# Kernel optimization log

Measured on AMD Instinct MI355X. Metric: run time of the kernel, lower is better.

The kernel has to match this reference:

```python
import jax, jax.numpy as jnp
import numpy as np

LAMDA = 1.0  # init arg: weight on uniformity term
ALIGN_ALPHA = 2.0
UNIF_T = 2.0
EPS = 1e-12


def _l2_normalize(x):
    # F.normalize(x, dim=1): x / max(||x||, eps)
    n = jnp.sqrt(jnp.sum(x * x, axis=1, keepdims=True))
    return x / jnp.maximum(n, EPS)


def _lalign(q, k):
    # mean over batch of ||q_i - k_i||_2 ^ alpha (alpha=2 -> squared distance)
    d2 = jnp.sum((q - k) ** 2, axis=1)
    return jnp.mean(d2)


def _lunif(x):
    # log( mean_{i<j} exp(-t * ||x_i - x_j||^2) )
    # x is unit-norm, so ||x_i - x_j||^2 = 2 - 2 <x_i, x_j>
    n = x.shape[0]
    sq = jnp.maximum(2.0 - 2.0 * (x @ x.T), 0.0)            # [N, N] squared dists
    iu = jnp.triu(jnp.ones((n, n), dtype=bool), k=1)        # strict upper: i < j pairs
    vals = jnp.where(iu, jnp.exp(-UNIF_T * sq), 0.0)
    npairs = jnp.asarray(n * (n - 1) // 2, dtype=x.dtype)
    return jnp.log(vals.sum() / npairs)


def setup_inputs() -> dict:
    key = jax.random.key(0)
    kq, kk = jax.random.split(key)
    q = jax.random.normal(kq, (8192, 128), dtype=jnp.float32)
    k = jax.random.normal(kk, (8192, 128), dtype=jnp.float32)
    return {"q": q, "k": k}


def reference(q, k):
    qn = _l2_normalize(q)
    kn = _l2_normalize(k)
    align = _lalign(qn, kn)
    uniform = (_lunif(qn) + _lunif(kn)) / 2.0
    return align + LAMDA * uniform
```

## Files before the change

### kernel.cpp

```cpp
#include <hip/hip_runtime.h>
#include <math.h>

#define NROWS 8192
#define DIM   128
#define NT    64
#define TRI   2080

typedef __attribute__((ext_vector_type(8))) __bf16 bf16x8;
typedef __attribute__((ext_vector_type(4))) float  f32x4;
typedef __attribute__((ext_vector_type(2))) float  f32x2;

__device__ __forceinline__ unsigned short f2bf(float f) {
    unsigned int u = __float_as_uint(f);
    u += 0x7fffu + ((u >> 16) & 1u);
    return (unsigned short)(u >> 16);
}

__device__ __forceinline__ void gload_lds16(const uint4* g, uint4* l) {
    __builtin_amdgcn_global_load_lds(
        (const __attribute__((address_space(1))) uint32_t*)
            (const __attribute__((address_space(1))) void*)g,
        (__attribute__((address_space(3))) uint32_t*)
            (__attribute__((address_space(3))) void*)l,
        16, 0, 0);
}

__global__ __launch_bounds__(256) void norm_kernel(
        const float* __restrict__ q, const float* __restrict__ k,
        unsigned int* __restrict__ qn, unsigned int* __restrict__ kn,
        float* __restrict__ align_part) {
    int wave = threadIdx.x >> 6;
    int lane = threadIdx.x & 63;
    int row  = blockIdx.x * 4 + wave;

    const float2 qv = reinterpret_cast<const float2*>(q)[row * 64 + lane];
    const float2 kv = reinterpret_cast<const float2*>(k)[row * 64 + lane];

    float sq = qv.x * qv.x + qv.y * qv.y;
    float sk = kv.x * kv.x + kv.y * kv.y;
    #pragma unroll
    for (int off = 32; off; off >>= 1) {
        sq += __shfl_xor(sq, off);
        sk += __shfl_xor(sk, off);
    }
    float qi = 1.0f / fmaxf(sqrtf(sq), 1e-12f);
    float ki = 1.0f / fmaxf(sqrtf(sk), 1e-12f);
    float qx = qv.x * qi, qy = qv.y * qi;
    float kx = kv.x * ki, ky = kv.y * ki;

    qn[row * 64 + lane] = (unsigned int)f2bf(qx) | ((unsigned int)f2bf(qy) << 16);
    kn[row * 64 + lane] = (unsigned int)f2bf(kx) | ((unsigned int)f2bf(ky) << 16);

    float dx = qx - kx, dy = qy - ky;
    float d2 = dx * dx + dy * dy;
    #pragma unroll
    for (int off = 32; off; off >>= 1) d2 += __shfl_xor(d2, off);

    __shared__ float red[4];
    if (lane == 0) red[wave] = d2;
    __syncthreads();
    if (threadIdx.x == 0)
        align_part[blockIdx.x] = red[0] + red[1] + red[2] + red[3];
}

__global__ __launch_bounds__(512) void gram_kernel(
        const uint4* __restrict__ qn, const uint4* __restrict__ kn,
        float* __restrict__ unif_part) {
    __shared__ uint4 lds[4096];
    __shared__ float red[8];

    int bid = blockIdx.x;
    int mat = 0, t = bid;
    if (t >= TRI) { mat = 1; t -= TRI; }
    int ti = 0, rem = t;
    while (rem >= NT - ti) { rem -= NT - ti; ++ti; }
    int tj = ti + rem;
    const uint4* __restrict__ x = mat ? kn : qn;

    int tid = threadIdx.x;
    int wid = tid >> 6, lane = tid & 63;

    {
        int lrow4 = lane >> 4;
        int sw    = lane & 15;
        #pragma unroll
        for (int it = 0; it < 8; ++it) {
            int inst = wid * 8 + it;
            int r    = inst * 4 + lrow4;
            int rr   = r & 127;
            int tile = (r < 128) ? ti : tj;
            int s    = sw ^ (rr & 15);
            gload_lds16(&x[((size_t)tile * 128 + rr) * 16 + s], &lds[inst * 64]);
        }
    }
    __syncthreads();

    int wr = wid >> 2, wc = wid & 3;
    int lr = lane & 15, lg = lane >> 4;

    f32x4 c[4][2];
    #pragma unroll
    for (int m = 0; m < 4; ++m)
        #pragma unroll
        for (int n = 0; n < 2; ++n)
            c[m][n] = (f32x4){0.f, 0.f, 0.f, 0.f};

    #pragma unroll
    for (int ks = 0; ks < 4; ++ks) {
        int slot = ks * 4 + lg;
        bf16x8 a[4], b[2];
        #pragma unroll
        for (int m = 0; m < 4; ++m) {
            int r = wr * 64 + m * 16 + lr;
            a[m] = *reinterpret_cast<const bf16x8*>(&lds[r * 16 + (slot ^ (r & 15))]);
        }
        #pragma unroll
        for (int n = 0; n < 2; ++n) {
            int r = wc * 32 + n * 16 + lr;
            b[n] = *reinterpret_cast<const bf16x8*>(&lds[2048 + r * 16 + (slot ^ (r & 15))]);
        }
        #pragma unroll
        for (int m = 0; m < 4; ++m)
            #pragma unroll
            for (int n = 0; n < 2; ++n)
                c[m][n] = __builtin_amdgcn_mfma_f32_16x16x32_bf16(a[m], b[n], c[m][n], 0, 0, 0);
    }

    const float K1 = 4.0f * 1.4426950408889634f * 8388608.0f;
    const float B  = 1065353216.0f - 0.05744f * 8388608.0f;
    const float K0 = B - K1;
    bool diag = (ti == tj);
    float psum = 0.0f;
    if (!diag) {
        f32x2 acc2 = (f32x2){0.f, 0.f};
        #pragma unroll
        for (int m = 0; m < 4; ++m)
            #pragma unroll
            for (int n = 0; n < 2; ++n) {
                f32x4 g = c[m][n];
                f32x2 u0 = (f32x2){g[0], g[1]} * K1 + K0;
                f32x2 u1 = (f32x2){g[2], g[3]} * K1 + K0;
                f32x2 e0 = (f32x2){__int_as_float((int)u0.x),
                                   __int_as_float((int)u0.y)};
                f32x2 e1 = (f32x2){__int_as_float((int)u1.x),
                                   __int_as_float((int)u1.y)};
                acc2 += e0;
                acc2 += e1;
            }
        psum = acc2.x + acc2.y;
    } else {
        int crow0 = wr * 64 + lg * 4;
        int ccol0 = wc * 32 + lr;
        #pragma unroll
        for (int m = 0; m < 4; ++m)
            #pragma unroll
            for (int n = 0; n < 2; ++n)
                #pragma unroll
                for (int r = 0; r < 4; ++r) {
                    float u = fminf(fmaf(c[m][n][r], K1, K0), B);
                    float e = __int_as_float((int)u);
                    int lrow = crow0 + m * 16 + r;
                    int lcol = ccol0 + n * 16;
                    psum += (lcol > lrow) ? e : 0.0f;
                }
    }
    #pragma unroll
    for (int off = 32; off; off >>= 1) psum += __shfl_xor(psum, off);

    if (lane == 0) red[wid] = psum;
    __syncthreads();
    if (tid == 0) {
        float s = 0.0f;
        #pragma unroll
        for (int w = 0; w < 8; ++w) s += red[w];
        unif_part[bid] = s;
    }
}

__global__ __launch_bounds__(256) void finalize(
        const float* __restrict__ align_part,
        const float* __restrict__ unif_part,
        float* __restrict__ out) {
    int tid = threadIdx.x;
    double a = 0.0, qs = 0.0, ks = 0.0;
    for (int i = tid; i < 2048; i += 256) a  += (double)align_part[i];
    for (int i = tid; i < TRI;  i += 256) qs += (double)unif_part[i];
    for (int i = tid; i < TRI;  i += 256) ks += (double)unif_part[TRI + i];

    __shared__ double sa[256], sq[256], sk[256];
    sa[tid] = a; sq[tid] = qs; sk[tid] = ks;
    __syncthreads();
    for (int s = 128; s; s >>= 1) {
        if (tid < s) {
            sa[tid] += sa[tid + s];
            sq[tid] += sq[tid + s];
            sk[tid] += sk[tid + s];
        }
        __syncthreads();
    }
    if (tid == 0) {
        const double npairs = (double)NROWS * (NROWS - 1) / 2.0;
        double align = sa[0] / (double)NROWS;
        double lq = log(sq[0] / npairs);
        double lk = log(sk[0] / npairs);
        out[0] = (float)(align + 0.5 * (lq + lk));
    }
}

extern "C" void kernel_launch(void* const* d_in, const int* in_sizes, int n_in,
                              void* d_out, int out_size, void* d_ws, size_t ws_size,
                              hipStream_t stream) {
    const float* q = (const float*)d_in[0];
    const float* k = (const float*)d_in[1];
    char* ws = (char*)d_ws;
    unsigned int* qn = (unsigned int*)ws;
    unsigned int* kn = (unsigned int*)(ws + (size_t)2 * 1024 * 1024);
    float* align_part = (float*)(ws + (size_t)4 * 1024 * 1024);
    float* unif_part  = (float*)(ws + (size_t)4 * 1024 * 1024 + 16384);
    float* out = (float*)d_out;

    norm_kernel<<<NROWS / 4, 256, 0, stream>>>(q, k, qn, kn, align_part);
    gram_kernel<<<2 * TRI, 512, 0, stream>>>((const uint4*)qn, (const uint4*)kn, unif_part);
    finalize<<<1, 256, 0, stream>>>(align_part, unif_part, out);
}
```

Measured before the change: 99.61 us.

## Make gram kernel persistent with double-buffered LDS tile prefetch

The gram kernel now launches a fixed 256-block persistent grid. Each block loops over triangle tiles with a stride and prefetches the next tile's rows into a second LDS buffer while computing the current one. Tile indices are decoded with a closed-form square-root formula instead of a loop. Per-block q and k partial sums are kept in registers and written once, which shrinks finalize's work. The costs are doubled LDS use (128KB per block), lower occupancy, and possible load imbalance across blocks, since tiles are assigned statically.

```diff
diff --git a/kernel.cpp b/kernel.cpp
--- a/kernel.cpp
+++ b/kernel.cpp
@@ -2,9 +2,10 @@
 #include <math.h>
 
 #define NROWS 8192
-#define DIM   128
 #define NT    64
 #define TRI   2080
+#define NTILE (2*TRI)
+#define GRID  256
 
 typedef __attribute__((ext_vector_type(8))) __bf16 bf16x8;
 typedef __attribute__((ext_vector_type(4))) float  f32x4;
@@ -25,6 +26,22 @@
         16, 0, 0);
 }
 
+__device__ __forceinline__ void decode_tile(int t, int& mat, int& ti, int& tj) {
+    mat = 0;
+    if (t >= TRI) { mat = 1; t -= TRI; }
+    float disc = (2.0f * NT + 1.0f) * (2.0f * NT + 1.0f) - 8.0f * (float)t;
+    int i = (int)(((2.0f * NT + 1.0f) - sqrtf(disc)) * 0.5f);
+    if (i < 0) i = 0;
+    if (i > NT - 1) i = NT - 1;
+    #pragma unroll
+    for (int f = 0; f < 2; ++f) {
+        if (i > 0 && (i * NT - i * (i - 1) / 2) > t) --i;
+        if (((i + 1) * NT - (i + 1) * i / 2) <= t) ++i;
+    }
+    ti = i;
+    tj = i + (t - (i * NT - i * (i - 1) / 2));
+}
+
 __global__ __launch_bounds__(256) void norm_kernel(
         const float* __restrict__ q, const float* __restrict__ k,
         unsigned int* __restrict__ qn, unsigned int* __restrict__ kn,
@@ -65,127 +82,147 @@
 
 __global__ __launch_bounds__(512) void gram_kernel(
         const uint4* __restrict__ qn, const uint4* __restrict__ kn,
-        float* __restrict__ unif_part) {
-    __shared__ uint4 lds[4096];
-    __shared__ float red[8];
-
-    int bid = blockIdx.x;
-    int mat = 0, t = bid;
-    if (t >= TRI) { mat = 1; t -= TRI; }
-    int ti = 0, rem = t;
-    while (rem >= NT - ti) { rem -= NT - ti; ++ti; }
-    int tj = ti + rem;
-    const uint4* __restrict__ x = mat ? kn : qn;
+        float* __restrict__ unif_q, float* __restrict__ unif_k) {
+    __shared__ uint4 lds[2][4096];
+    __shared__ float redq[8], redk[8];
 
     int tid = threadIdx.x;
     int wid = tid >> 6, lane = tid & 63;
-
-    {
-        int lrow4 = lane >> 4;
-        int sw    = lane & 15;
-        #pragma unroll
-        for (int it = 0; it < 8; ++it) {
-            int inst = wid * 8 + it;
-            int r    = inst * 4 + lrow4;
-            int rr   = r & 127;
-            int tile = (r < 128) ? ti : tj;
-            int s    = sw ^ (rr & 15);
-            gload_lds16(&x[((size_t)tile * 128 + rr) * 16 + s], &lds[inst * 64]);
-        }
-    }
-    __syncthreads();
-
     int wr = wid >> 2, wc = wid & 3;
     int lr = lane & 15, lg = lane >> 4;
-
-    f32x4 c[4][2];
-    #pragma unroll
-    for (int m = 0; m < 4; ++m)
-        #pragma unroll
-        for (int n = 0; n < 2; ++n)
-            c[m][n] = (f32x4){0.f, 0.f, 0.f, 0.f};
-
-    #pragma unroll
-    for (int ks = 0; ks < 4; ++ks) {
-        int slot = ks * 4 + lg;
-        bf16x8 a[4], b[2];
-        #pragma unroll
-        for (int m = 0; m < 4; ++m) {
-            int r = wr * 64 + m * 16 + lr;
-            a[m] = *reinterpret_cast<const bf16x8*>(&lds[r * 16 + (slot ^ (r & 15))]);
-        }
-        #pragma unroll
-        for (int n = 0; n < 2; ++n) {
-            int r = wc * 32 + n * 16 + lr;
-            b[n] = *reinterpret_cast<const bf16x8*>(&lds[2048 + r * 16 + (slot ^ (r & 15))]);
-        }
-        #pragma unroll
-        for (int m = 0; m < 4; ++m)
-            #pragma unroll
-            for (int n = 0; n < 2; ++n)
-                c[m][n] = __builtin_amdgcn_mfma_f32_16x16x32_bf16(a[m], b[n], c[m][n], 0, 0, 0);
-    }
 
     const float K1 = 4.0f * 1.4426950408889634f * 8388608.0f;
     const float B  = 1065353216.0f - 0.05744f * 8388608.0f;
     const float K0 = B - K1;
-    bool diag = (ti == tj);
-    float psum = 0.0f;
-    if (!diag) {
-        f32x2 acc2 = (f32x2){0.f, 0.f};
+
+    auto stage = [&](uint4* buf, int mat, int ti, int tj) {
+        const uint4* __restrict__ x = mat ? kn : qn;
+        #pragma unroll
+        for (int it = 0; it < 8; ++it) {
+            int inst = wid * 8 + it;
+            int li   = inst * 64 + lane;
+            int rr   = li >> 4, s = li & 15;
+            int tile = (rr < 128) ? ti : tj;
+            int r7   = rr & 127;
+            int ss   = s ^ (rr & 15);
+            gload_lds16(&x[((size_t)tile * 128 + r7) * 16 + ss], &buf[inst * 64]);
+        }
+    };
+
+    f32x2 aq2 = (f32x2){0.f, 0.f}, ak2 = (f32x2){0.f, 0.f};
+
+    int t = blockIdx.x;
+    int cmat, cti, ctj;
+    decode_tile(t, cmat, cti, ctj);
+    stage(lds[0], cmat, cti, ctj);
+    __syncthreads();
+    int cur = 0;
+
+    while (t < NTILE) {
+        int tn = t + GRID;
+        int nmat = 0, nti = 0, ntj = 0;
+        if (tn < NTILE) {
+            decode_tile(tn, nmat, nti, ntj);
+            stage(lds[cur ^ 1], nmat, nti, ntj);
+        }
+
+        const uint4* bufA = &lds[cur][0];
+        const uint4* bufB = &lds[cur][2048];
+
+        f32x4 c[4][2];
         #pragma unroll
         for (int m = 0; m < 4; ++m)
             #pragma unroll
+            for (int n = 0; n < 2; ++n)
+                c[m][n] = (f32x4){0.f, 0.f, 0.f, 0.f};
+
+        #pragma unroll
+        for (int ks = 0; ks < 4; ++ks) {
+            int slot = ks * 4 + lg;
+            bf16x8 a[4], b[2];
+            #pragma unroll
+            for (int m = 0; m < 4; ++m) {
+                int r = wr * 64 + m * 16 + lr;
+                a[m] = *reinterpret_cast<const bf16x8*>(&bufA[r * 16 + (slot ^ (r & 15))]);
+            }
+            #pragma unroll
             for (int n = 0; n < 2; ++n) {
-                f32x4 g = c[m][n];
-                f32x2 u0 = (f32x2){g[0], g[1]} * K1 + K0;
-                f32x2 u1 = (f32x2){g[2], g[3]} * K1 + K0;
-                f32x2 e0 = (f32x2){__int_as_float((int)u0.x),
-                                   __int_as_float((int)u0.y)};
-                f32x2 e1 = (f32x2){__int_as_float((int)u1.x),
-                                   __int_as_float((int)u1.y)};
-                acc2 += e0;
-                acc2 += e1;
+                int r = wc * 32 + n * 16 + lr;
+                b[n] = *reinterpret_cast<const bf16x8*>(&bufB[r * 16 + (slot ^ (r & 15))]);
             }
-        psum = acc2.x + acc2.y;
-    } else {
-        int crow0 = wr * 64 + lg * 4;
-        int ccol0 = wc * 32 + lr;
-        #pragma unroll
-        for (int m = 0; m < 4; ++m)
-            #pragma unroll
-            for (int n = 0; n < 2; ++n)
+            #pragma unroll
+            for (int m = 0; m < 4; ++m)
                 #pragma unroll
-                for (int r = 0; r < 4; ++r) {
-                    float u = fminf(fmaf(c[m][n][r], K1, K0), B);
-                    float e = __int_as_float((int)u);
-                    int lrow = crow0 + m * 16 + r;
-                    int lcol = ccol0 + n * 16;
-                    psum += (lcol > lrow) ? e : 0.0f;
+                for (int n = 0; n < 2; ++n)
+                    c[m][n] = __builtin_amdgcn_mfma_f32_16x16x32_bf16(a[m], b[n], c[m][n], 0, 0, 0);
+        }
+
+        f32x2 p2 = (f32x2){0.f, 0.f};
+        if (cti != ctj) {
+            #pragma unroll
+            for (int m = 0; m < 4; ++m)
+                #pragma unroll
+                for (int n = 0; n < 2; ++n) {
+                    f32x4 g = c[m][n];
+                    f32x2 u0 = (f32x2){g[0], g[1]} * K1 + K0;
+                    f32x2 u1 = (f32x2){g[2], g[3]} * K1 + K0;
+                    p2 += (f32x2){__int_as_float((int)u0.x),
+                                  __int_as_float((int)u0.y)};
+                    p2 += (f32x2){__int_as_float((int)u1.x),
+                                  __int_as_float((int)u1.y)};
                 }
-    }
-    #pragma unroll
-    for (int off = 32; off; off >>= 1) psum += __shfl_xor(psum, off);
-
-    if (lane == 0) red[wid] = psum;
+        } else {
+            int crow0 = wr * 64 + lg * 4;
+            int ccol0 = wc * 32 + lr;
+            float ps = 0.0f;
+            #pragma unroll
+            for (int m = 0; m < 4; ++m)
+                #pragma unroll
+                for (int n = 0; n < 2; ++n)
+                    #pragma unroll
+                    for (int r = 0; r < 4; ++r) {
+                        float uu = fminf(fmaf(c[m][n][r], K1, K0), B);
+                        float e = __int_as_float((int)uu);
+                        int lrow = crow0 + m * 16 + r;
+                        int lcol = ccol0 + n * 16;
+                        ps += (lcol > lrow) ? e : 0.0f;
+                    }
+            p2.x = ps;
+        }
+        if (cmat) ak2 += p2; else aq2 += p2;
+
+        __syncthreads();
+        cur ^= 1;
+        t = tn;
+        cmat = nmat; cti = nti; ctj = ntj;
+    }
+
+    float pq = aq2.x + aq2.y, pk = ak2.x + ak2.y;
+    #pragma unroll
+    for (int off = 32; off; off >>= 1) {
+        pq += __shfl_xor(pq, off);
+        pk += __shfl_xor(pk, off);
+    }
+    if (lane == 0) { redq[wid] = pq; redk[wid] = pk; }
     __syncthreads();
     if (tid == 0) {
-        float s = 0.0f;
-        #pragma unroll
-        for (int w = 0; w < 8; ++w) s += red[w];
-        unif_part[bid] = s;
+        float sq = 0.0f, sk = 0.0f;
+        #pragma unroll
+        for (int w = 0; w < 8; ++w) { sq += redq[w]; sk += redk[w]; }
+        unif_q[blockIdx.x] = sq;
+        unif_k[blockIdx.x] = sk;
     }
 }
 
 __global__ __launch_bounds__(256) void finalize(
         const float* __restrict__ align_part,
-        const float* __restrict__ unif_part,
+        const float* __restrict__ unif_q,
+        const float* __restrict__ unif_k,
         float* __restrict__ out) {
     int tid = threadIdx.x;
     double a = 0.0, qs = 0.0, ks = 0.0;
-    for (int i = tid; i < 2048; i += 256) a  += (double)align_part[i];
-    for (int i = tid; i < TRI;  i += 256) qs += (double)unif_part[i];
-    for (int i = tid; i < TRI;  i += 256) ks += (double)unif_part[TRI + i];
+    for (int i = tid; i < 2048; i += 256) a += (double)align_part[i];
+    if (tid < GRID) { qs = (double)unif_q[tid]; ks = (double)unif_k[tid]; }
 
     __shared__ double sa[256], sq[256], sk[256];
     sa[tid] = a; sq[tid] = qs; sk[tid] = ks;
@@ -216,10 +253,11 @@
     unsigned int* qn = (unsigned int*)ws;
     unsigned int* kn = (unsigned int*)(ws + (size_t)2 * 1024 * 1024);
     float* align_part = (float*)(ws + (size_t)4 * 1024 * 1024);
-    float* unif_part  = (float*)(ws + (size_t)4 * 1024 * 1024 + 16384);
+    float* unif_q = (float*)(ws + (size_t)4 * 1024 * 1024 + 16384);
+    float* unif_k = (float*)(ws + (size_t)4 * 1024 * 1024 + 32768);
     float* out = (float*)d_out;
 
     norm_kernel<<<NROWS / 4, 256, 0, stream>>>(q, k, qn, kn, align_part);
-    gram_kernel<<<2 * TRI, 512, 0, stream>>>((const uint4*)qn, (const uint4*)kn, unif_part);
-    finalize<<<1, 256, 0, stream>>>(align_part, unif_part, out);
-}
+    gram_kernel<<<GRID, 512, 0, stream>>>((const uint4*)qn, (const uint4*)kn, unif_q, unif_k);
+    finalize<<<1, 256, 0, stream>>>(align_part, unif_q, unif_k, out);
+}
```

Result: faster. 97.50 us (-2.1%).
